# Kernel optimization log

Measured on AMD Instinct MI355X. Metric: run time of the kernel, lower is better.

Reference implementation:

```python
import jax, jax.numpy as jnp
import numpy as np

N_A, N_B = 50000, 200000          # coarse / fine active voxel counts
C_A, C_B, C_OUT = 256, 128, 256   # channels: x_a, x_b (skip), output
K_T, M_T = 8, 100000              # transpose conv: 2^3 offsets, pairs per offset
K_C, M_C = 27, 120000             # 3x3x3 conv: 27 offsets, pairs per offset
EPS = 1e-5


def setup_inputs() -> dict:
    key = jax.random.key(0)
    ks = jax.random.split(key, 12)
    feats_a = jax.random.normal(ks[0], (N_A, C_A), jnp.float32)
    feats_b = jax.random.normal(ks[1], (N_B, C_B), jnp.float32)
    W_t = jax.random.normal(ks[2], (K_T, C_A, C_A), jnp.float32) * 0.05
    W_c = jax.random.normal(ks[3], (K_C, C_A + C_B, C_OUT), jnp.float32) * 0.05
    in_map_t = jax.random.randint(ks[4], (K_T, M_T), 0, N_A, dtype=jnp.int32)
    out_map_t = jax.random.randint(ks[5], (K_T, M_T), 0, N_B, dtype=jnp.int32)
    in_map_c = jax.random.randint(ks[6], (K_C, M_C), 0, N_B, dtype=jnp.int32)
    out_map_c = jax.random.randint(ks[7], (K_C, M_C), 0, N_B, dtype=jnp.int32)
    bn_t_gamma = jax.random.uniform(ks[8], (C_A,), jnp.float32, 0.5, 1.5)
    bn_t_beta = jax.random.normal(ks[9], (C_A,), jnp.float32) * 0.1
    bn_t_mean = jax.random.normal(ks[10], (C_A,), jnp.float32) * 0.1
    bn_t_var = jax.random.uniform(ks[11], (C_A,), jnp.float32, 0.5, 1.5)
    k2 = jax.random.split(jax.random.key(1), 4)
    bn_c_gamma = jax.random.uniform(k2[0], (C_OUT,), jnp.float32, 0.5, 1.5)
    bn_c_beta = jax.random.normal(k2[1], (C_OUT,), jnp.float32) * 0.1
    bn_c_mean = jax.random.normal(k2[2], (C_OUT,), jnp.float32) * 0.1
    bn_c_var = jax.random.uniform(k2[3], (C_OUT,), jnp.float32, 0.5, 1.5)
    return {
        "feats_a": feats_a, "feats_b": feats_b,
        "W_t": W_t, "bn_t_gamma": bn_t_gamma, "bn_t_beta": bn_t_beta,
        "bn_t_mean": bn_t_mean, "bn_t_var": bn_t_var,
        "W_c": W_c, "bn_c_gamma": bn_c_gamma, "bn_c_beta": bn_c_beta,
        "bn_c_mean": bn_c_mean, "bn_c_var": bn_c_var,
        "in_map_t": in_map_t, "out_map_t": out_map_t,
        "in_map_c": in_map_c, "out_map_c": out_map_c,
    }


def _sparse_conv(feats, in_map, out_map, W, n_out):
    """MinkowskiEngine gather-GEMM-scatter over kernel maps.
    feats: [N_in, C_in]; in_map/out_map: [K, M] index pairs per kernel offset;
    W: [K, C_in, C_out]. Scan over the K offsets (small fixed set) to keep
    peak memory at one [M, C] slab."""
    acc0 = jnp.zeros((n_out, W.shape[-1]), feats.dtype)

    def step(acc, kmaps):
        im, om, Wk = kmaps
        acc = acc.at[om].add(feats[im] @ Wk)  # gather -> GEMM -> scatter-add
        return acc, None

    out, _ = jax.lax.scan(step, acc0, (in_map, out_map, W))
    return out


def _bn_relu(x, gamma, beta, mean, var):
    # BatchNorm in eval mode (running stats) + ReLU
    return jax.nn.relu((x - mean) * (gamma / jnp.sqrt(var + EPS)) + beta)


def reference(feats_a, feats_b, W_t, bn_t_gamma, bn_t_beta, bn_t_mean, bn_t_var,
              W_c, bn_c_gamma, bn_c_beta, bn_c_mean, bn_c_var,
              in_map_t, out_map_t, in_map_c, out_map_c):
    # conv_a: transpose conv (k=2, s=2) -> BN -> ReLU; output lives on x_b coords
    xa = _sparse_conv(feats_a, in_map_t, out_map_t, W_t, N_B)
    xa = _bn_relu(xa, bn_t_gamma, bn_t_beta, bn_t_mean, bn_t_var)
    # ME.cat: concatenate features at identical coordinates
    x = jnp.concatenate([xa, feats_b], axis=-1)  # [N_B, C_A + C_B]
    # conv_proj: 3x3x3 conv -> BN -> ReLU
    x = _sparse_conv(x, in_map_c, out_map_c, W_c, N_B)
    return _bn_relu(x, bn_c_gamma, bn_c_beta, bn_c_mean, bn_c_var)
```

## Files before the change

kernel.cpp:

```cpp
#include <hip/hip_runtime.h>
#include <hip/hip_bf16.h>
#include <stdint.h>

typedef __attribute__((ext_vector_type(8))) short bf16x8;
typedef __attribute__((ext_vector_type(4))) float floatx4;

#define DEV __device__ __forceinline__

DEV void gl_lds16(const void* g, void* lds) {
    __builtin_amdgcn_global_load_lds(
        (const __attribute__((address_space(1))) unsigned int*)g,
        (__attribute__((address_space(3))) unsigned int*)lds, 16, 0, 0);
}

template <int KSTEPS>
__global__ __launch_bounds__(256) void spconv_kernel(
    const __hip_bfloat16* __restrict__ A, const __hip_bfloat16* __restrict__ BT,
    const int* __restrict__ in_map, const int* __restrict__ out_map,
    float* __restrict__ Out, int M) {
    constexpr int K = KSTEPS * 32;
    __shared__ __align__(16) char Abuf[8192];
    __shared__ __align__(16) char Bbuf[8192];
    __shared__ int om_s[128];

    const int tid = threadIdx.x;
    const int w = tid >> 6;
    const int l = tid & 63;
    const int koff = blockIdx.z;
    const int m0 = blockIdx.x * 128;
    const int n0 = blockIdx.y * 128;

    const int* im = in_map + (size_t)koff * M;
    const int* om = out_map + (size_t)koff * M;

    if (tid < 128) {
        int p = m0 + tid;
        om_s[tid] = (p < M) ? om[p] : -1;
    }

    const int rS = (w & 1) * 64 + l;
    int prow = m0 + rS;
    if (prow > M - 1) prow = M - 1;
    const __hip_bfloat16* a_row = A + (size_t)im[prow] * K;
    const __hip_bfloat16* b_row = BT + ((size_t)koff * 256 + n0 + rS) * (size_t)K;
    const int q0 = w >> 1;

    char* Al = Abuf + w * 1024 + l * 16;
    char* Bl = Bbuf + w * 1024 + l * 16;

    floatx4 acc[4][4];
#pragma unroll
    for (int i = 0; i < 4; i++)
#pragma unroll
        for (int j = 0; j < 4; j++) acc[i][j] = (floatx4)0.0f;

    const int wm = w & 1, wn = w >> 1;
    const int lm = l & 15, lq = l >> 4;

    for (int ks = 0; ks < KSTEPS; ks++) {
        const int kb = ks * 32;
        gl_lds16(a_row + kb + q0 * 8, Al);
        gl_lds16(a_row + kb + (q0 + 2) * 8, Al + 4096);
        gl_lds16(b_row + kb + q0 * 8, Bl);
        gl_lds16(b_row + kb + (q0 + 2) * 8, Bl + 4096);
        __syncthreads();

        bf16x8 af[4], bf[4];
#pragma unroll
        for (int mt = 0; mt < 4; mt++)
            af[mt] = *(const bf16x8*)(Abuf + lq * 2048 + (wm * 64 + mt * 16 + lm) * 16);
#pragma unroll
        for (int nt = 0; nt < 4; nt++)
            bf[nt] = *(const bf16x8*)(Bbuf + lq * 2048 + (wn * 64 + nt * 16 + lm) * 16);

#pragma unroll
        for (int mt = 0; mt < 4; mt++)
#pragma unroll
            for (int nt = 0; nt < 4; nt++)
                acc[mt][nt] = __builtin_amdgcn_mfma_f32_16x16x32_bf16(
                    af[mt], bf[nt], acc[mt][nt], 0, 0, 0);

        __syncthreads();
    }

#pragma unroll
    for (int mt = 0; mt < 4; mt++) {
        const int mbase = wm * 64 + mt * 16 + lq * 4;
#pragma unroll
        for (int r = 0; r < 4; r++) {
            const int orow = om_s[mbase + r];
            if (orow >= 0) {
                float* dst = Out + (size_t)orow * 256 + n0 + wn * 64 + lm;
#pragma unroll
                for (int nt = 0; nt < 4; nt++)
                    unsafeAtomicAdd(dst + nt * 16, acc[mt][nt][r]);
            }
        }
    }
}

struct __align__(8) bf4 { __hip_bfloat16 h[4]; };

__global__ void cast_bf16_kernel(const float* __restrict__ in,
                                 __hip_bfloat16* __restrict__ out, int n4) {
    int stride = gridDim.x * blockDim.x;
    for (int i = blockIdx.x * blockDim.x + threadIdx.x; i < n4; i += stride) {
        float4 v = ((const float4*)in)[i];
        bf4 o;
        o.h[0] = __float2bfloat16(v.x);
        o.h[1] = __float2bfloat16(v.y);
        o.h[2] = __float2bfloat16(v.z);
        o.h[3] = __float2bfloat16(v.w);
        ((bf4*)out)[i] = o;
    }
}

__global__ void transpose_cast_w(const float* __restrict__ W,
                                 __hip_bfloat16* __restrict__ WT, int Koff,
                                 int Cin, int Cout) {
    int total = Koff * Cin * Cout;
    int stride = gridDim.x * blockDim.x;
    for (int i = blockIdx.x * blockDim.x + threadIdx.x; i < total; i += stride) {
        int k = i / (Cin * Cout);
        int r = i - k * (Cin * Cout);
        int n = r / Cin;
        int kk = r - n * Cin;
        WT[i] = __float2bfloat16(W[((size_t)k * Cin + kk) * Cout + n]);
    }
}

__global__ void bn_concat_kernel(const float* __restrict__ xa,
                                 const float* __restrict__ fb,
                                 const float* __restrict__ g,
                                 const float* __restrict__ b,
                                 const float* __restrict__ mu,
                                 const float* __restrict__ var,
                                 __hip_bfloat16* __restrict__ X) {
    const int total = 200000 * 96;
    int stride = gridDim.x * blockDim.x;
    for (int i = blockIdx.x * blockDim.x + threadIdx.x; i < total; i += stride) {
        int row = i / 96;
        int c4 = (i - row * 96) * 4;
        float v[4];
        if (c4 < 256) {
            float4 t = *(const float4*)(xa + (size_t)row * 256 + c4);
            v[0] = t.x; v[1] = t.y; v[2] = t.z; v[3] = t.w;
#pragma unroll
            for (int j = 0; j < 4; j++) {
                int c = c4 + j;
                float s = g[c] * rsqrtf(var[c] + 1e-5f);
                v[j] = fmaxf((v[j] - mu[c]) * s + b[c], 0.0f);
            }
        } else {
            float4 t = *(const float4*)(fb + (size_t)row * 128 + (c4 - 256));
            v[0] = t.x; v[1] = t.y; v[2] = t.z; v[3] = t.w;
        }
        bf4 o;
#pragma unroll
        for (int j = 0; j < 4; j++) o.h[j] = __float2bfloat16(v[j]);
        *(bf4*)(X + (size_t)row * 384 + c4) = o;
    }
}

__global__ void bn_out_kernel(float* __restrict__ out, const float* __restrict__ g,
                              const float* __restrict__ b,
                              const float* __restrict__ mu,
                              const float* __restrict__ var) {
    const int total = 200000 * 64;
    int stride = gridDim.x * blockDim.x;
    for (int i = blockIdx.x * blockDim.x + threadIdx.x; i < total; i += stride) {
        int c4 = (i & 63) * 4;
        float4 t = ((const float4*)out)[i];
        float v[4] = {t.x, t.y, t.z, t.w};
#pragma unroll
        for (int j = 0; j < 4; j++) {
            int c = c4 + j;
            float s = g[c] * rsqrtf(var[c] + 1e-5f);
            v[j] = fmaxf((v[j] - mu[c]) * s + b[c], 0.0f);
        }
        ((float4*)out)[i] = make_float4(v[0], v[1], v[2], v[3]);
    }
}

extern "C" void kernel_launch(void* const* d_in, const int* in_sizes, int n_in,
                              void* d_out, int out_size, void* d_ws,
                              size_t ws_size, hipStream_t stream) {
    const float* feats_a = (const float*)d_in[0];
    const float* feats_b = (const float*)d_in[1];
    const float* W_t = (const float*)d_in[2];
    const float* bn_t_gamma = (const float*)d_in[3];
    const float* bn_t_beta = (const float*)d_in[4];
    const float* bn_t_mean = (const float*)d_in[5];
    const float* bn_t_var = (const float*)d_in[6];
    const float* W_c = (const float*)d_in[7];
    const float* bn_c_gamma = (const float*)d_in[8];
    const float* bn_c_beta = (const float*)d_in[9];
    const float* bn_c_mean = (const float*)d_in[10];
    const float* bn_c_var = (const float*)d_in[11];
    const int* in_map_t = (const int*)d_in[12];
    const int* out_map_t = (const int*)d_in[13];
    const int* in_map_c = (const int*)d_in[14];
    const int* out_map_c = (const int*)d_in[15];
    float* out = (float*)d_out;

    char* ws = (char*)d_ws;
    __hip_bfloat16* a_bf = (__hip_bfloat16*)ws;
    __hip_bfloat16* wtT = (__hip_bfloat16*)(ws + 25600000);
    __hip_bfloat16* wcT = (__hip_bfloat16*)(ws + 26648576);
    __hip_bfloat16* x_bf = (__hip_bfloat16*)(ws + 31956992);

    cast_bf16_kernel<<<512, 256, 0, stream>>>(feats_a, a_bf, 50000 * 256 / 4);
    transpose_cast_w<<<512, 256, 0, stream>>>(W_t, wtT, 8, 256, 256);
    transpose_cast_w<<<512, 256, 0, stream>>>(W_c, wcT, 27, 384, 256);

    hipMemsetAsync(d_out, 0, (size_t)out_size * sizeof(float), stream);
    dim3 g1(782, 2, 8);
    spconv_kernel<8><<<g1, 256, 0, stream>>>(a_bf, wtT, in_map_t, out_map_t, out, 100000);

    bn_concat_kernel<<<2048, 256, 0, stream>>>(out, feats_b, bn_t_gamma, bn_t_beta,
                                               bn_t_mean, bn_t_var, x_bf);

    hipMemsetAsync(d_out, 0, (size_t)out_size * sizeof(float), stream);
    dim3 g2(938, 2, 27);
    spconv_kernel<12><<<g2, 256, 0, stream>>>(x_bf, wcT, in_map_c, out_map_c, out, 120000);

    bn_out_kernel<<<2048, 256, 0, stream>>>(out, bn_c_gamma, bn_c_beta, bn_c_mean,
                                            bn_c_var);
}
```

Before: 4.000 ms.

## Triple-buffer LDS tiles to overlap global loads with MFMA compute

Replaces the single LDS buffer (load, sync, compute, sync each K-step) with a 3-stage ring of A/B buffers. Loads for step k+2 are issued before computing step k, with manual vmcnt waits and one barrier per step. The aim is to hide gather latency behind MFMA work. LDS use triples to about 48KB per block, which may lower occupancy, and the correctness of the manual waitcnt depends on the om_s store and im load ordering.

```diff
diff --git a/kernel.cpp b/kernel.cpp
--- a/kernel.cpp
+++ b/kernel.cpp
@@ -12,6 +12,14 @@
         (const __attribute__((address_space(1))) unsigned int*)g,
         (__attribute__((address_space(3))) unsigned int*)lds, 16, 0, 0);
 }
+
+#define WAIT_VM4() asm volatile("s_waitcnt vmcnt(4)" ::: "memory")
+#define WAIT_VM0() asm volatile("s_waitcnt vmcnt(0)" ::: "memory")
+#define BAR()                              \
+    do {                                   \
+        __builtin_amdgcn_s_barrier();      \
+        asm volatile("" ::: "memory");     \
+    } while (0)
 
 template <int KSTEPS>
 __global__ __launch_bounds__(256) void spconv_kernel(
@@ -19,8 +27,8 @@
     const int* __restrict__ in_map, const int* __restrict__ out_map,
     float* __restrict__ Out, int M) {
     constexpr int K = KSTEPS * 32;
-    __shared__ __align__(16) char Abuf[8192];
-    __shared__ __align__(16) char Bbuf[8192];
+    __shared__ __align__(16) char Abuf[3][8192];
+    __shared__ __align__(16) char Bbuf[3][8192];
     __shared__ int om_s[128];
 
     const int tid = threadIdx.x;
@@ -41,12 +49,12 @@
     const int rS = (w & 1) * 64 + l;
     int prow = m0 + rS;
     if (prow > M - 1) prow = M - 1;
-    const __hip_bfloat16* a_row = A + (size_t)im[prow] * K;
-    const __hip_bfloat16* b_row = BT + ((size_t)koff * 256 + n0 + rS) * (size_t)K;
-    const int q0 = w >> 1;
-
-    char* Al = Abuf + w * 1024 + l * 16;
-    char* Bl = Bbuf + w * 1024 + l * 16;
+    const char* a_src = (const char*)(A + (size_t)im[prow] * K);
+    const char* b_src =
+        (const char*)(BT + ((size_t)koff * 256 + n0 + rS) * (size_t)K);
+    const int so0 = (w >> 1) * 16;
+    const int so1 = so0 + 32;
+    const int dA = w * 1024 + l * 16;
 
     floatx4 acc[4][4];
 #pragma unroll
@@ -57,31 +65,48 @@
     const int wm = w & 1, wn = w >> 1;
     const int lm = l & 15, lq = l >> 4;
 
-    for (int ks = 0; ks < KSTEPS; ks++) {
-        const int kb = ks * 32;
-        gl_lds16(a_row + kb + q0 * 8, Al);
-        gl_lds16(a_row + kb + (q0 + 2) * 8, Al + 4096);
-        gl_lds16(b_row + kb + q0 * 8, Bl);
-        gl_lds16(b_row + kb + (q0 + 2) * 8, Bl + 4096);
-        __syncthreads();
-
+    auto stage = [&](int buf, int ks) {
+        const int kb = ks * 64;
+        gl_lds16(a_src + kb + so0, &Abuf[buf][dA]);
+        gl_lds16(a_src + kb + so1, &Abuf[buf][dA + 4096]);
+        gl_lds16(b_src + kb + so0, &Bbuf[buf][dA]);
+        gl_lds16(b_src + kb + so1, &Bbuf[buf][dA + 4096]);
+    };
+
+    auto compute = [&](int buf) {
         bf16x8 af[4], bf[4];
 #pragma unroll
         for (int mt = 0; mt < 4; mt++)
-            af[mt] = *(const bf16x8*)(Abuf + lq * 2048 + (wm * 64 + mt * 16 + lm) * 16);
+            af[mt] = *(const bf16x8*)(&Abuf[buf][lq * 2048 +
+                                                 (wm * 64 + mt * 16 + lm) * 16]);
 #pragma unroll
         for (int nt = 0; nt < 4; nt++)
-            bf[nt] = *(const bf16x8*)(Bbuf + lq * 2048 + (wn * 64 + nt * 16 + lm) * 16);
-
+            bf[nt] = *(const bf16x8*)(&Bbuf[buf][lq * 2048 +
+                                                 (wn * 64 + nt * 16 + lm) * 16]);
 #pragma unroll
         for (int mt = 0; mt < 4; mt++)
 #pragma unroll
             for (int nt = 0; nt < 4; nt++)
                 acc[mt][nt] = __builtin_amdgcn_mfma_f32_16x16x32_bf16(
                     af[mt], bf[nt], acc[mt][nt], 0, 0, 0);
-
-        __syncthreads();
-    }
+    };
+
+    static_assert(KSTEPS >= 3, "pipeline needs >=3 K-steps");
+    stage(0, 0);
+    stage(1, 1);
+
+    for (int ks = 0; ks < KSTEPS - 2; ks++) {
+        WAIT_VM4();
+        BAR();
+        stage((ks + 2) % 3, ks + 2);
+        compute(ks % 3);
+    }
+    WAIT_VM4();
+    BAR();
+    compute((KSTEPS - 2) % 3);
+    WAIT_VM0();
+    BAR();
+    compute((KSTEPS - 1) % 3);
 
 #pragma unroll
     for (int mt = 0; mt < 4; mt++) {
```

After: 3.917 ms. 2.1% less time.
